# Kernel optimization log

Hardware: AMD Instinct MI355X
Metric: run time of the kernel (lower is better)

Reference implementation:

```python
import jax, jax.numpy as jnp
import numpy as np

WS = 16      # window size
NH = 8       # num heads
LN_EPS = 1e-5
F_NORM_EPS = 1e-12  # torch F.normalize eps


def layer_norm(x, w, b):
    mu = jnp.mean(x, axis=-1, keepdims=True)
    var = jnp.mean((x - mu) ** 2, axis=-1, keepdims=True)
    return (x - mu) / jnp.sqrt(var + LN_EPS) * w + b


def setup_inputs() -> dict:
    key = jax.random.key(0)
    ks = jax.random.split(key, 8)
    b, h, w, c = 2, 192, 192, 128
    n = WS * WS
    x = jax.random.normal(ks[0], (b, h * w, c), dtype=jnp.float32)
    rpi = jax.random.randint(ks[1], (n, n), 0, (2 * WS - 1) ** 2)
    s = 0.02
    inp = {
        'x': x,
        'qkv_w': jax.random.normal(ks[2], (c, 3 * c), jnp.float32) * s,
        'qkv_b': jnp.zeros((3 * c,), jnp.float32),
        'proj_w': jax.random.normal(ks[3], (c, c), jnp.float32) * s,
        'proj_b': jnp.zeros((c,), jnp.float32),
        'logit_scale': jnp.full((NH, 1, 1), jnp.log(10.0), jnp.float32),
        'rpb_table': jax.random.normal(ks[4], ((2 * WS - 1) ** 2, NH), jnp.float32) * s,
        'norm1_w': jnp.ones((c,), jnp.float32),
        'norm1_b': jnp.zeros((c,), jnp.float32),
        'norm2_w': jnp.ones((c,), jnp.float32),
        'norm2_b': jnp.zeros((c,), jnp.float32),
        'fc1_w': jax.random.normal(ks[5], (c, 2 * c), jnp.float32) * s,
        'fc1_b': jnp.zeros((2 * c,), jnp.float32),
        'fc2_w': jax.random.normal(ks[6], (2 * c, c), jnp.float32) * s,
        'fc2_b': jnp.zeros((c,), jnp.float32),
        'h': h,
        'w': w,
        'rpi': rpi,
    }
    return inp


def reference(x, qkv_w, qkv_b, proj_w, proj_b, logit_scale, rpb_table,
              norm1_w, norm1_b, norm2_w, norm2_b, fc1_w, fc1_b, fc2_w, fc2_b,
              h, w, rpi):
    b, L, c = x.shape
    ws, nh = WS, NH
    d = c // nh
    n = ws * ws
    shortcut = x

    # window partition: (b, h, w, c) -> (b*nW, ws*ws, c)
    xi = x.reshape(b, h // ws, ws, w // ws, ws, c)
    xw = xi.transpose(0, 1, 3, 2, 4, 5).reshape(-1, n, c)

    # cosine window attention (SwinV2 style)
    qkv = (xw @ qkv_w + qkv_b).reshape(-1, n, 3, nh, d).transpose(2, 0, 3, 1, 4)
    q, k, v = qkv[0], qkv[1], qkv[2]                       # (B_, nh, n, d)
    qn = q / jnp.maximum(jnp.linalg.norm(q, axis=-1, keepdims=True), F_NORM_EPS)
    kn = k / jnp.maximum(jnp.linalg.norm(k, axis=-1, keepdims=True), F_NORM_EPS)
    scale = jnp.exp(jnp.minimum(logit_scale, jnp.log(100.0)))  # (nh,1,1)
    attn = jnp.einsum('bhnd,bhmd->bhnm', qn, kn) * scale
    bias = rpb_table[rpi.reshape(-1)].reshape(n, n, nh).transpose(2, 0, 1)
    attn = jax.nn.softmax(attn + bias[None], axis=-1)
    out = jnp.einsum('bhnm,bhmd->bhnd', attn, v)
    out = out.transpose(0, 2, 1, 3).reshape(-1, n, c) @ proj_w + proj_b

    # window reverse
    xr = out.reshape(b, h // ws, w // ws, ws, ws, c)
    xr = xr.transpose(0, 1, 3, 2, 4, 5).reshape(b, L, c)

    # res-post-norm residual + MLP (GELU), eval mode (no dropout/drop_path)
    x1 = shortcut + layer_norm(xr, norm1_w, norm1_b)
    y = jax.nn.gelu(x1 @ fc1_w + fc1_b, approximate=False) @ fc2_w + fc2_b
    return x1 + layer_norm(y, norm2_w, norm2_b)
```

## Files before the change

kernel.cpp:

```cpp
#include <hip/hip_runtime.h>
#include <hip/hip_bf16.h>
#include <math.h>

#define BB 2
#define HH 192
#define WW 192
#define CC 128
#define LL (HH*WW)
#define WSZ 16
#define NTOK 256
#define NHEAD 8
#define DHEAD 16
#define NWS 12
#define NWB 144
#define NWT 288
#define MT (BB*LL)
#define LOG2E 1.44269504088896340736f

#define OFF_BIAS   0
#define OFF_QKV    262144
#define OFF_ATTN   14417920
#define OFF_X1     19136512
#define OFF_X1B    28573696
#define OFF_HID    33292288
#define OFF_WT     42729472
#define WT_QKV 0
#define WT_PROJ 49152
#define WT_FC1 65536
#define WT_FC2 98304

typedef short  bf16x8  __attribute__((ext_vector_type(8)));
typedef short  bf16x4  __attribute__((ext_vector_type(4)));
typedef float  f32x4   __attribute__((ext_vector_type(4)));
typedef float  f32x16  __attribute__((ext_vector_type(16)));
typedef uint   uint4v  __attribute__((ext_vector_type(4)));
#define MFMA16(a,b,c) __builtin_amdgcn_mfma_f32_16x16x32_bf16(a,b,c,0,0,0)
#define MFMA32(a,b,c) __builtin_amdgcn_mfma_f32_32x32x16_bf16(a,b,c,0,0,0)

__device__ __forceinline__ ushort f2b(float f) {
    uint u = __float_as_uint(f);
    uint r = u + 0x7fffu + ((u >> 16) & 1u);
    return (ushort)(r >> 16);
}
__device__ __forceinline__ uint pk(float a, float b) {
    return (uint)f2b(a) | ((uint)f2b(b) << 16);
}
__device__ __forceinline__ float b2f(ushort u) {
    return __uint_as_float(((uint)u) << 16);
}

__device__ __forceinline__ int win_to_g(int wi, int t) {
    int b   = wi / NWB;
    int win = wi - b*NWB;
    int hi  = win / NWS;
    int wj  = win - hi*NWS;
    return b*LL + (hi*WSZ + (t >> 4))*WW + wj*WSZ + (t & 15);
}

__global__ __launch_bounds__(256) void bias_kernel(const int* __restrict__ rpi,
                                                   const float* __restrict__ rpb,
                                                   ushort* __restrict__ biasT) {
    int gid = blockIdx.x*256 + threadIdx.x;
    int q = gid >> 8, k = gid & 255;
    int idx = rpi[q*256 + k];
    #pragma unroll
    for (int h = 0; h < 8; ++h)
        biasT[h*65536 + q*256 + k] = f2b(rpb[idx*8 + h] * LOG2E);
}

__global__ __launch_bounds__(256) void wconv_kernel(const float* __restrict__ qkv_w,
                                                    const float* __restrict__ proj_w,
                                                    const float* __restrict__ fc1_w,
                                                    const float* __restrict__ fc2_w,
                                                    ushort* __restrict__ wt) {
    int gid = blockIdx.x*256 + threadIdx.x;
    if (gid < 49152) {
        int n = gid >> 7, k = gid & 127;
        wt[gid] = f2b(qkv_w[k*384 + n]);
    } else if (gid < 65536) {
        int i = gid - 49152; int n = i >> 7, k = i & 127;
        wt[gid] = f2b(proj_w[k*128 + n]);
    } else if (gid < 98304) {
        int i = gid - 65536; int n = i >> 7, k = i & 127;
        wt[gid] = f2b(fc1_w[k*256 + n]);
    } else {
        int i = gid - 98304; int n = i >> 8, k = i & 255;
        wt[gid] = f2b(fc2_w[k*128 + n]);
    }
}

__global__ __launch_bounds__(256) void qkv_mfma(const float* __restrict__ x,
                                                const ushort* __restrict__ wt,
                                                const float* __restrict__ wb,
                                                const float* __restrict__ lscale,
                                                ushort* __restrict__ qkvbuf) {
    __shared__ ushort alds[128][136];
    const int tid = threadIdx.x;
    const int wi  = blockIdx.x >> 1;
    const int t0w = (blockIdx.x & 1) << 7;
    #pragma unroll
    for (int it = 0; it < 16; ++it) {
        int idx = it*256 + tid;
        int row = idx >> 5, c4 = idx & 31;
        int g = win_to_g(wi, t0w + row);
        float4 v = ((const float4*)x)[g*32 + c4];
        ushort4 b;
        b.x = f2b(v.x); b.y = f2b(v.y); b.z = f2b(v.z); b.w = f2b(v.w);
        *(ushort4*)&alds[row][c4*4] = b;
    }
    __syncthreads();
    const int wv = tid >> 6, lane = tid & 63;
    const int lr = lane & 15, kg = lane >> 4;
    bf16x8 af[2][4];
    #pragma unroll
    for (int mt = 0; mt < 2; ++mt)
        #pragma unroll
        for (int ks = 0; ks < 4; ++ks)
            af[mt][ks] = *(const bf16x8*)&alds[wv*32 + mt*16 + lr][ks*32 + kg*8];

    #pragma unroll 4
    for (int t = 0; t < 24; ++t) {
        bf16x8 bfr[4];
        #pragma unroll
        for (int ks = 0; ks < 4; ++ks)
            bfr[ks] = *(const bf16x8*)(wt + (t*16 + lr)*128 + ks*32 + kg*8);
        f32x4 acc[2];
        acc[0] = (f32x4)0.f; acc[1] = (f32x4)0.f;
        #pragma unroll
        for (int mt = 0; mt < 2; ++mt)
            #pragma unroll
            for (int ks = 0; ks < 4; ++ks)
                acc[mt] = MFMA16(af[mt][ks], bfr[ks], acc[mt]);

        const int s = t >> 3, head = t & 7;
        const float bcol = wb[s*128 + head*16 + lr];
        #pragma unroll
        for (int mt = 0; mt < 2; ++mt)
            #pragma unroll
            for (int r = 0; r < 4; ++r) acc[mt][r] += bcol;
        if (s < 2) {
            float sc = (s == 0) ? __expf(fminf(lscale[head], 4.6051701860f)) * LOG2E : 1.f;
            #pragma unroll
            for (int mt = 0; mt < 2; ++mt)
                #pragma unroll
                for (int r = 0; r < 4; ++r) {
                    float ss = acc[mt][r]*acc[mt][r];
                    ss += __shfl_xor(ss, 1);
                    ss += __shfl_xor(ss, 2);
                    ss += __shfl_xor(ss, 4);
                    ss += __shfl_xor(ss, 8);
                    acc[mt][r] *= sc / fmaxf(sqrtf(ss), 1e-12f);
                }
        }
        ushort* dst = qkvbuf + ((wi*8+head)*3 + s)*4096;
        #pragma unroll
        for (int mt = 0; mt < 2; ++mt)
            #pragma unroll
            for (int r = 0; r < 4; ++r) {
                int row = t0w + wv*32 + mt*16 + kg*4 + r;
                dst[row*16 + lr] = f2b(acc[mt][r]);
            }
    }
}

__global__ __launch_bounds__(256) void attn_mfma(const ushort* __restrict__ qkv,
                                                 const ushort* __restrict__ biasT,
                                                 ushort* __restrict__ attn_o) {
    __shared__ ushort Vt[16][260];
    __shared__ float  ltab[4][2][32];
    const int tid = threadIdx.x;
    const int wi = blockIdx.x >> 3, head = blockIdx.x & 7;
    const ushort* qb = qkv + ((wi*8 + head)*3)*4096;
    const ushort* kb = qb + 4096;
    const ushort* vb = qb + 8192;
    {
        const ushort* vr = vb + tid*16;
        #pragma unroll
        for (int c = 0; c < 4; ++c) {
            ushort4 vv = *(const ushort4*)(vr + c*4);
            Vt[c*4+0][tid] = vv.x; Vt[c*4+1][tid] = vv.y;
            Vt[c*4+2][tid] = vv.z; Vt[c*4+3][tid] = vv.w;
        }
    }
    const int wv = tid >> 6, lane = tid & 63;
    const int l31 = lane & 31, hi = lane >> 5;
    const int dp = l31 & 15;
    bf16x8 qf[2];
    #pragma unroll
    for (int mt = 0; mt < 2; ++mt)
        qf[mt] = *(const bf16x8*)(qb + (wv*64 + mt*32 + l31)*16 + hi*8);
    const ushort* brow0 = biasT + head*65536 + (wv*64 + l31)*256;
    __syncthreads();

    f32x16 oacc[2];
    oacc[0] = (f32x16)0.f; oacc[1] = (f32x16)0.f;
    float lsum0 = 0.f, lsum1 = 0.f;

    for (int kt = 0; kt < 8; ++kt) {
        bf16x8 kf = *(const bf16x8*)(kb + (kt*32 + l31)*16 + hi*8);
        #pragma unroll
        for (int mt = 0; mt < 2; ++mt) {
            f32x16 s = MFMA32(kf, qf[mt], (f32x16)0.f);
            const ushort* br = brow0 + mt*32*256 + kt*32 + 4*hi;
            ushort4 b0 = *(const ushort4*)(br + 0);
            ushort4 b1 = *(const ushort4*)(br + 8);
            ushort4 b2 = *(const ushort4*)(br + 16);
            ushort4 b3 = *(const ushort4*)(br + 24);
            float p[16];
            p[0]  = exp2f(s[0]  + b2f(b0.x));
            p[1]  = exp2f(s[1]  + b2f(b0.y));
            p[2]  = exp2f(s[2]  + b2f(b0.z));
            p[3]  = exp2f(s[3]  + b2f(b0.w));
            p[4]  = exp2f(s[4]  + b2f(b1.x));
            p[5]  = exp2f(s[5]  + b2f(b1.y));
            p[6]  = exp2f(s[6]  + b2f(b1.z));
            p[7]  = exp2f(s[7]  + b2f(b1.w));
            p[8]  = exp2f(s[8]  + b2f(b2.x));
            p[9]  = exp2f(s[9]  + b2f(b2.y));
            p[10] = exp2f(s[10] + b2f(b2.z));
            p[11] = exp2f(s[11] + b2f(b2.w));
            p[12] = exp2f(s[12] + b2f(b3.x));
            p[13] = exp2f(s[13] + b2f(b3.y));
            p[14] = exp2f(s[14] + b2f(b3.z));
            p[15] = exp2f(s[15] + b2f(b3.w));
            float ls = ((p[0]+p[1])+(p[2]+p[3])) + ((p[4]+p[5])+(p[6]+p[7]))
                     + ((p[8]+p[9])+(p[10]+p[11])) + ((p[12]+p[13])+(p[14]+p[15]));
            if (mt == 0) lsum0 += ls; else lsum1 += ls;
            uint4v t0 = { pk(p[0],p[1]),  pk(p[2],p[3]),  pk(p[4],p[5]),  pk(p[6],p[7])  };
            uint4v t1 = { pk(p[8],p[9]),  pk(p[10],p[11]),pk(p[12],p[13]),pk(p[14],p[15])};
            bf16x8 pf0 = __builtin_bit_cast(bf16x8, t0);
            bf16x8 pf1 = __builtin_bit_cast(bf16x8, t1);
            bf16x4 v00 = *(const bf16x4*)&Vt[dp][kt*32 + hi*4];
            bf16x4 v01 = *(const bf16x4*)&Vt[dp][kt*32 + 8 + hi*4];
            bf16x4 v10 = *(const bf16x4*)&Vt[dp][kt*32 + 16 + hi*4];
            bf16x4 v11 = *(const bf16x4*)&Vt[dp][kt*32 + 24 + hi*4];
            bf16x8 vf0 = __builtin_shufflevector(v00, v01, 0,1,2,3,4,5,6,7);
            bf16x8 vf1 = __builtin_shufflevector(v10, v11, 0,1,2,3,4,5,6,7);
            oacc[mt] = MFMA32(pf0, vf0, oacc[mt]);
            oacc[mt] = MFMA32(pf1, vf1, oacc[mt]);
        }
    }
    {
        float t0 = lsum0 + __shfl_xor(lsum0, 32);
        float t1 = lsum1 + __shfl_xor(lsum1, 32);
        ltab[wv][0][l31] = 1.f / t0;
        ltab[wv][1][l31] = 1.f / t1;
    }
    __syncthreads();
    if (l31 < 16) {
        #pragma unroll
        for (int mt = 0; mt < 2; ++mt) {
            #pragma unroll
            for (int i = 0; i < 16; ++i) {
                int q = (i&3) + 8*(i>>2) + 4*hi;
                float il = ltab[wv][mt][q];
                attn_o[(wi*256 + wv*64 + mt*32 + q)*128 + head*16 + l31]
                    = f2b(oacc[mt][i] * il);
            }
        }
    }
}

__global__ __launch_bounds__(256) void proj_mfma(const ushort* __restrict__ a,
                                                 const ushort* __restrict__ wt,
                                                 const float* __restrict__ wb,
                                                 const float* __restrict__ x,
                                                 const float* __restrict__ n1w,
                                                 const float* __restrict__ n1b,
                                                 float* __restrict__ x1,
                                                 ushort* __restrict__ x1b) {
    __shared__ ushort alds[128][136];
    const int tid = threadIdx.x;
    const int M0 = blockIdx.x * 128;
    #pragma unroll
    for (int it = 0; it < 16; ++it) {
        int idx = it*256 + tid;
        int row = idx >> 5, c4 = idx & 31;
        *(ushort4*)&alds[row][c4*4] = ((const ushort4*)a)[M0*32 + idx];
    }
    __syncthreads();
    const int wv = tid >> 6, lane = tid & 63;
    const int lr = lane & 15, kg = lane >> 4;
    bf16x8 af[2][4];
    #pragma unroll
    for (int mt = 0; mt < 2; ++mt)
        #pragma unroll
        for (int ks = 0; ks < 4; ++ks)
            af[mt][ks] = *(const bf16x8*)&alds[wv*32 + mt*16 + lr][ks*32 + kg*8];

    f32x4 acc[2][8];
    #pragma unroll
    for (int mt = 0; mt < 2; ++mt)
        #pragma unroll
        for (int t = 0; t < 8; ++t) acc[mt][t] = (f32x4)0.f;
    #pragma unroll
    for (int t = 0; t < 8; ++t) {
        bf16x8 bfr[4];
        #pragma unroll
        for (int ks = 0; ks < 4; ++ks)
            bfr[ks] = *(const bf16x8*)(wt + (t*16 + lr)*128 + ks*32 + kg*8);
        #pragma unroll
        for (int mt = 0; mt < 2; ++mt)
            #pragma unroll
            for (int ks = 0; ks < 4; ++ks)
                acc[mt][t] = MFMA16(af[mt][ks], bfr[ks], acc[mt][t]);
    }
    #pragma unroll
    for (int t = 0; t < 8; ++t) {
        float bcol = wb[t*16 + lr];
        #pragma unroll
        for (int mt = 0; mt < 2; ++mt)
            #pragma unroll
            for (int r = 0; r < 4; ++r) acc[mt][t][r] += bcol;
    }
    float mu_[2][4], rs_[2][4];
    #pragma unroll
    for (int mt = 0; mt < 2; ++mt)
        #pragma unroll
        for (int r = 0; r < 4; ++r) {
            float s = 0.f, q = 0.f;
            #pragma unroll
            for (int t = 0; t < 8; ++t) { float v = acc[mt][t][r]; s += v; q += v*v; }
            s += __shfl_xor(s,1); q += __shfl_xor(q,1);
            s += __shfl_xor(s,2); q += __shfl_xor(q,2);
            s += __shfl_xor(s,4); q += __shfl_xor(q,4);
            s += __shfl_xor(s,8); q += __shfl_xor(q,8);
            float mu = s*(1.f/128.f);
            float var = q*(1.f/128.f) - mu*mu;
            mu_[mt][r] = mu; rs_[mt][r] = rsqrtf(var + 1e-5f);
        }
    float w1c[8], b1c[8];
    #pragma unroll
    for (int t = 0; t < 8; ++t) { w1c[t] = n1w[t*16+lr]; b1c[t] = n1b[t*16+lr]; }
    #pragma unroll
    for (int mt = 0; mt < 2; ++mt)
        #pragma unroll
        for (int r = 0; r < 4; ++r) {
            int M = M0 + wv*32 + mt*16 + kg*4 + r;
            int g = win_to_g(M >> 8, M & 255);
            #pragma unroll
            for (int t = 0; t < 8; ++t) {
                int col = t*16 + lr;
                float val = x[g*128 + col]
                          + (acc[mt][t][r]-mu_[mt][r])*rs_[mt][r]*w1c[t] + b1c[t];
                x1[g*128 + col] = val;
                x1b[g*128 + col] = f2b(val);
            }
        }
}

__global__ __launch_bounds__(256) void fc1_mfma(const ushort* __restrict__ a,
                                                const ushort* __restrict__ wt,
                                                const float* __restrict__ wb,
                                                ushort* __restrict__ hidden) {
    __shared__ ushort alds[128][136];
    const int tid = threadIdx.x;
    const int M0 = blockIdx.x * 128;
    #pragma unroll
    for (int it = 0; it < 16; ++it) {
        int idx = it*256 + tid;
        int row = idx >> 5, c4 = idx & 31;
        *(ushort4*)&alds[row][c4*4] = ((const ushort4*)a)[M0*32 + idx];
    }
    __syncthreads();
    const int wv = tid >> 6, lane = tid & 63;
    const int lr = lane & 15, kg = lane >> 4;
    bf16x8 af[2][4];
    #pragma unroll
    for (int mt = 0; mt < 2; ++mt)
        #pragma unroll
        for (int ks = 0; ks < 4; ++ks)
            af[mt][ks] = *(const bf16x8*)&alds[wv*32 + mt*16 + lr][ks*32 + kg*8];

    #pragma unroll 4
    for (int t = 0; t < 16; ++t) {
        bf16x8 bfr[4];
        #pragma unroll
        for (int ks = 0; ks < 4; ++ks)
            bfr[ks] = *(const bf16x8*)(wt + (t*16 + lr)*128 + ks*32 + kg*8);
        f32x4 acc[2];
        acc[0] = (f32x4)0.f; acc[1] = (f32x4)0.f;
        #pragma unroll
        for (int mt = 0; mt < 2; ++mt)
            #pragma unroll
            for (int ks = 0; ks < 4; ++ks)
                acc[mt] = MFMA16(af[mt][ks], bfr[ks], acc[mt]);
        float bcol = wb[t*16 + lr];
        int col = t*16 + lr;
        #pragma unroll
        for (int mt = 0; mt < 2; ++mt)
            #pragma unroll
            for (int r = 0; r < 4; ++r) {
                int row = M0 + wv*32 + mt*16 + kg*4 + r;
                float v = acc[mt][r] + bcol;
                float gl = v*0.5f*(1.f + erff(v*0.70710678118654752f));
                hidden[row*256 + col] = f2b(gl);
            }
    }
}

__global__ __launch_bounds__(256) void fc2_mfma(const ushort* __restrict__ a,
                                                const ushort* __restrict__ wt,
                                                const float* __restrict__ wb,
                                                const float* __restrict__ x1,
                                                const float* __restrict__ n2w,
                                                const float* __restrict__ n2b,
                                                float* __restrict__ out) {
    __shared__ ushort alds[128][136];
    const int tid = threadIdx.x;
    const int M0 = blockIdx.x * 128;
    const int wv = tid >> 6, lane = tid & 63;
    const int lr = lane & 15, kg = lane >> 4;
    f32x4 acc[2][8];
    #pragma unroll
    for (int mt = 0; mt < 2; ++mt)
        #pragma unroll
        for (int t = 0; t < 8; ++t) acc[mt][t] = (f32x4)0.f;

    for (int ko = 0; ko < 2; ++ko) {
        if (ko) __syncthreads();
        #pragma unroll
        for (int it = 0; it < 16; ++it) {
            int idx = it*256 + tid;
            int row = idx >> 5, c4 = idx & 31;
            *(ushort4*)&alds[row][c4*4] =
                *(const ushort4*)(a + (M0+row)*256 + ko*128 + c4*4);
        }
        __syncthreads();
        bf16x8 af[2][4];
        #pragma unroll
        for (int mt = 0; mt < 2; ++mt)
            #pragma unroll
            for (int ks = 0; ks < 4; ++ks)
                af[mt][ks] = *(const bf16x8*)&alds[wv*32 + mt*16 + lr][ks*32 + kg*8];
        #pragma unroll
        for (int t = 0; t < 8; ++t) {
            bf16x8 bfr[4];
            #pragma unroll
            for (int ks = 0; ks < 4; ++ks)
                bfr[ks] = *(const bf16x8*)(wt + (t*16 + lr)*256 + ko*128 + ks*32 + kg*8);
            #pragma unroll
            for (int mt = 0; mt < 2; ++mt)
                #pragma unroll
                for (int ks = 0; ks < 4; ++ks)
                    acc[mt][t] = MFMA16(af[mt][ks], bfr[ks], acc[mt][t]);
        }
    }
    #pragma unroll
    for (int t = 0; t < 8; ++t) {
        float bcol = wb[t*16 + lr];
        #pragma unroll
        for (int mt = 0; mt < 2; ++mt)
            #pragma unroll
            for (int r = 0; r < 4; ++r) acc[mt][t][r] += bcol;
    }
    float mu_[2][4], rs_[2][4];
    #pragma unroll
    for (int mt = 0; mt < 2; ++mt)
        #pragma unroll
        for (int r = 0; r < 4; ++r) {
            float s = 0.f, q = 0.f;
            #pragma unroll
            for (int t = 0; t < 8; ++t) { float v = acc[mt][t][r]; s += v; q += v*v; }
            s += __shfl_xor(s,1); q += __shfl_xor(q,1);
            s += __shfl_xor(s,2); q += __shfl_xor(q,2);
            s += __shfl_xor(s,4); q += __shfl_xor(q,4);
            s += __shfl_xor(s,8); q += __shfl_xor(q,8);
            float mu = s*(1.f/128.f);
            float var = q*(1.f/128.f) - mu*mu;
            mu_[mt][r] = mu; rs_[mt][r] = rsqrtf(var + 1e-5f);
        }
    float w2c[8], b2c[8];
    #pragma unroll
    for (int t = 0; t < 8; ++t) { w2c[t] = n2w[t*16+lr]; b2c[t] = n2b[t*16+lr]; }
    #pragma unroll
    for (int mt = 0; mt < 2; ++mt)
        #pragma unroll
        for (int r = 0; r < 4; ++r) {
            int g = M0 + wv*32 + mt*16 + kg*4 + r;
            #pragma unroll
            for (int t = 0; t < 8; ++t) {
                int col = t*16 + lr;
                out[g*128 + col] = x1[g*128 + col]
                                 + (acc[mt][t][r]-mu_[mt][r])*rs_[mt][r]*w2c[t] + b2c[t];
            }
        }
}

extern "C" void kernel_launch(void* const* d_in, const int* in_sizes, int n_in,
                              void* d_out, int out_size, void* d_ws, size_t ws_size,
                              hipStream_t stream) {
    const float* x      = (const float*)d_in[0];
    const float* qkv_w  = (const float*)d_in[1];
    const float* qkv_b  = (const float*)d_in[2];
    const float* proj_w = (const float*)d_in[3];
    const float* proj_b = (const float*)d_in[4];
    const float* lscale = (const float*)d_in[5];
    const float* rpb    = (const float*)d_in[6];
    const float* n1w    = (const float*)d_in[7];
    const float* n1b    = (const float*)d_in[8];
    const float* n2w    = (const float*)d_in[9];
    const float* n2b    = (const float*)d_in[10];
    const float* fc1_w  = (const float*)d_in[11];
    const float* fc1_b  = (const float*)d_in[12];
    const float* fc2_w  = (const float*)d_in[13];
    const float* fc2_b  = (const float*)d_in[14];
    const int*   rpi    = (const int*)d_in[17];
    float* out = (float*)d_out;

    float* ws      = (float*)d_ws;
    ushort* biasT  = (ushort*)(ws + OFF_BIAS);
    ushort* qkvbuf = (ushort*)(ws + OFF_QKV);
    ushort* attn_o = (ushort*)(ws + OFF_ATTN);
    float*  x1     = ws + OFF_X1;
    ushort* x1b    = (ushort*)(ws + OFF_X1B);
    ushort* hidden = (ushort*)(ws + OFF_HID);
    ushort* wt     = (ushort*)(ws + OFF_WT);

    bias_kernel<<<256, 256, 0, stream>>>(rpi, rpb, biasT);
    wconv_kernel<<<512, 256, 0, stream>>>(qkv_w, proj_w, fc1_w, fc2_w, wt);
    qkv_mfma<<<576, 256, 0, stream>>>(x, wt + WT_QKV, qkv_b, lscale, qkvbuf);
    attn_mfma<<<2304, 256, 0, stream>>>(qkvbuf, biasT, attn_o);
    proj_mfma<<<576, 256, 0, stream>>>(attn_o, wt + WT_PROJ, proj_b, x, n1w, n1b, x1, x1b);
    fc1_mfma<<<576, 256, 0, stream>>>(x1b, wt + WT_FC1, fc1_b, hidden);
    fc2_mfma<<<576, 256, 0, stream>>>(hidden, wt + WT_FC2, fc2_b, x1, n2w, n2b, out);
}
```

Baseline: 353.1 us.

## Fold bias into MFMA accumulator, compute row sums via ones-column, use hardware bf16 pack

The relative-position bias is now stored in fp32 and passed as the initial accumulator of the QK^T MFMA, which removes the per-element bias add. The softmax denominator is no longer summed on the VALU. A constant row of ones is appended to the V tile, so the idle upper lanes of the PV MFMA produce the row sums, which are then shuffled back to the output lanes. This also removes the LDS table and a barrier. Float-to-bf16 conversion switches to the v_cvt_pk_bf16_f32 instruction. In exchange the bias buffer is twice as large, so the attention kernel reads more global memory.

```diff
diff --git a/kernel.cpp b/kernel.cpp
--- a/kernel.cpp
+++ b/kernel.cpp
@@ -18,12 +18,12 @@
 #define LOG2E 1.44269504088896340736f
 
 #define OFF_BIAS   0
-#define OFF_QKV    262144
-#define OFF_ATTN   14417920
-#define OFF_X1     19136512
-#define OFF_X1B    28573696
-#define OFF_HID    33292288
-#define OFF_WT     42729472
+#define OFF_QKV    524288
+#define OFF_ATTN   14680064
+#define OFF_X1     19398656
+#define OFF_X1B    28835840
+#define OFF_HID    33554432
+#define OFF_WT     42991616
 #define WT_QKV 0
 #define WT_PROJ 49152
 #define WT_FC1 65536
@@ -37,13 +37,15 @@
 #define MFMA16(a,b,c) __builtin_amdgcn_mfma_f32_16x16x32_bf16(a,b,c,0,0,0)
 #define MFMA32(a,b,c) __builtin_amdgcn_mfma_f32_32x32x16_bf16(a,b,c,0,0,0)
 
+__device__ __forceinline__ uint cvtpk(float a, float b) {
+    uint r;
+    asm("v_cvt_pk_bf16_f32 %0, %1, %2" : "=v"(r) : "v"(a), "v"(b));
+    return r;
+}
 __device__ __forceinline__ ushort f2b(float f) {
-    uint u = __float_as_uint(f);
-    uint r = u + 0x7fffu + ((u >> 16) & 1u);
-    return (ushort)(r >> 16);
-}
-__device__ __forceinline__ uint pk(float a, float b) {
-    return (uint)f2b(a) | ((uint)f2b(b) << 16);
+    uint r;
+    asm("v_cvt_pk_bf16_f32 %0, %1, %1" : "=v"(r) : "v"(f));
+    return (ushort)r;
 }
 __device__ __forceinline__ float b2f(ushort u) {
     return __uint_as_float(((uint)u) << 16);
@@ -59,13 +61,13 @@
 
 __global__ __launch_bounds__(256) void bias_kernel(const int* __restrict__ rpi,
                                                    const float* __restrict__ rpb,
-                                                   ushort* __restrict__ biasT) {
+                                                   float* __restrict__ biasT) {
     int gid = blockIdx.x*256 + threadIdx.x;
     int q = gid >> 8, k = gid & 255;
     int idx = rpi[q*256 + k];
     #pragma unroll
     for (int h = 0; h < 8; ++h)
-        biasT[h*65536 + q*256 + k] = f2b(rpb[idx*8 + h] * LOG2E);
+        biasT[h*65536 + q*256 + k] = rpb[idx*8 + h] * LOG2E;
 }
 
 __global__ __launch_bounds__(256) void wconv_kernel(const float* __restrict__ qkv_w,
@@ -104,9 +106,10 @@
         int row = idx >> 5, c4 = idx & 31;
         int g = win_to_g(wi, t0w + row);
         float4 v = ((const float4*)x)[g*32 + c4];
-        ushort4 b;
-        b.x = f2b(v.x); b.y = f2b(v.y); b.z = f2b(v.z); b.w = f2b(v.w);
-        *(ushort4*)&alds[row][c4*4] = b;
+        uint2 pkd;
+        pkd.x = cvtpk(v.x, v.y);
+        pkd.y = cvtpk(v.z, v.w);
+        *(uint2*)&alds[row][c4*4] = pkd;
     }
     __syncthreads();
     const int wv = tid >> 6, lane = tid & 63;
@@ -164,10 +167,9 @@
 }
 
 __global__ __launch_bounds__(256) void attn_mfma(const ushort* __restrict__ qkv,
-                                                 const ushort* __restrict__ biasT,
+                                                 const float* __restrict__ biasT,
                                                  ushort* __restrict__ attn_o) {
-    __shared__ ushort Vt[16][260];
-    __shared__ float  ltab[4][2][32];
+    __shared__ ushort Vt[17][260];
     const int tid = threadIdx.x;
     const int wi = blockIdx.x >> 3, head = blockIdx.x & 7;
     const ushort* qb = qkv + ((wi*8 + head)*3)*4096;
@@ -181,53 +183,40 @@
             Vt[c*4+0][tid] = vv.x; Vt[c*4+1][tid] = vv.y;
             Vt[c*4+2][tid] = vv.z; Vt[c*4+3][tid] = vv.w;
         }
+        Vt[16][tid] = 0x3F80;
     }
     const int wv = tid >> 6, lane = tid & 63;
     const int l31 = lane & 31, hi = lane >> 5;
-    const int dp = l31 & 15;
+    const int dp = (l31 < 16) ? l31 : 16;
     bf16x8 qf[2];
     #pragma unroll
     for (int mt = 0; mt < 2; ++mt)
         qf[mt] = *(const bf16x8*)(qb + (wv*64 + mt*32 + l31)*16 + hi*8);
-    const ushort* brow0 = biasT + head*65536 + (wv*64 + l31)*256;
+    const float* brow0 = biasT + head*65536 + (wv*64 + l31)*256 + 4*hi;
     __syncthreads();
 
     f32x16 oacc[2];
     oacc[0] = (f32x16)0.f; oacc[1] = (f32x16)0.f;
-    float lsum0 = 0.f, lsum1 = 0.f;
 
     for (int kt = 0; kt < 8; ++kt) {
         bf16x8 kf = *(const bf16x8*)(kb + (kt*32 + l31)*16 + hi*8);
         #pragma unroll
         for (int mt = 0; mt < 2; ++mt) {
-            f32x16 s = MFMA32(kf, qf[mt], (f32x16)0.f);
-            const ushort* br = brow0 + mt*32*256 + kt*32 + 4*hi;
-            ushort4 b0 = *(const ushort4*)(br + 0);
-            ushort4 b1 = *(const ushort4*)(br + 8);
-            ushort4 b2 = *(const ushort4*)(br + 16);
-            ushort4 b3 = *(const ushort4*)(br + 24);
+            const float* br = brow0 + mt*8192 + kt*32;
+            float4 b0 = *(const float4*)(br);
+            float4 b1 = *(const float4*)(br + 8);
+            float4 b2 = *(const float4*)(br + 16);
+            float4 b3 = *(const float4*)(br + 24);
+            f32x16 ci = { b0.x,b0.y,b0.z,b0.w, b1.x,b1.y,b1.z,b1.w,
+                          b2.x,b2.y,b2.z,b2.w, b3.x,b3.y,b3.z,b3.w };
+            f32x16 s = MFMA32(kf, qf[mt], ci);
             float p[16];
-            p[0]  = exp2f(s[0]  + b2f(b0.x));
-            p[1]  = exp2f(s[1]  + b2f(b0.y));
-            p[2]  = exp2f(s[2]  + b2f(b0.z));
-            p[3]  = exp2f(s[3]  + b2f(b0.w));
-            p[4]  = exp2f(s[4]  + b2f(b1.x));
-            p[5]  = exp2f(s[5]  + b2f(b1.y));
-            p[6]  = exp2f(s[6]  + b2f(b1.z));
-            p[7]  = exp2f(s[7]  + b2f(b1.w));
-            p[8]  = exp2f(s[8]  + b2f(b2.x));
-            p[9]  = exp2f(s[9]  + b2f(b2.y));
-            p[10] = exp2f(s[10] + b2f(b2.z));
-            p[11] = exp2f(s[11] + b2f(b2.w));
-            p[12] = exp2f(s[12] + b2f(b3.x));
-            p[13] = exp2f(s[13] + b2f(b3.y));
-            p[14] = exp2f(s[14] + b2f(b3.z));
-            p[15] = exp2f(s[15] + b2f(b3.w));
-            float ls = ((p[0]+p[1])+(p[2]+p[3])) + ((p[4]+p[5])+(p[6]+p[7]))
-                     + ((p[8]+p[9])+(p[10]+p[11])) + ((p[12]+p[13])+(p[14]+p[15]));
-            if (mt == 0) lsum0 += ls; else lsum1 += ls;
-            uint4v t0 = { pk(p[0],p[1]),  pk(p[2],p[3]),  pk(p[4],p[5]),  pk(p[6],p[7])  };
-            uint4v t1 = { pk(p[8],p[9]),  pk(p[10],p[11]),pk(p[12],p[13]),pk(p[14],p[15])};
+            #pragma unroll
+            for (int i = 0; i < 16; ++i) p[i] = exp2f(s[i]);
+            uint4v t0 = { cvtpk(p[0],p[1]),   cvtpk(p[2],p[3]),
+                          cvtpk(p[4],p[5]),   cvtpk(p[6],p[7]) };
+            uint4v t1 = { cvtpk(p[8],p[9]),   cvtpk(p[10],p[11]),
+                          cvtpk(p[12],p[13]), cvtpk(p[14],p[15]) };
             bf16x8 pf0 = __builtin_bit_cast(bf16x8, t0);
             bf16x8 pf1 = __builtin_bit_cast(bf16x8, t1);
             bf16x4 v00 = *(const bf16x4*)&Vt[dp][kt*32 + hi*4];
@@ -240,20 +229,18 @@
             oacc[mt] = MFMA32(pf1, vf1, oacc[mt]);
         }
     }
-    {
-        float t0 = lsum0 + __shfl_xor(lsum0, 32);
-        float t1 = lsum1 + __shfl_xor(lsum1, 32);
-        ltab[wv][0][l31] = 1.f / t0;
-        ltab[wv][1][l31] = 1.f / t1;
-    }
-    __syncthreads();
-    if (l31 < 16) {
-        #pragma unroll
-        for (int mt = 0; mt < 2; ++mt) {
-            #pragma unroll
-            for (int i = 0; i < 16; ++i) {
+    #pragma unroll
+    for (int mt = 0; mt < 2; ++mt) {
+        f32x16 o = oacc[mt];
+        if (l31 >= 16) {
+            #pragma unroll
+            for (int i = 0; i < 16; ++i) o[i] = __builtin_amdgcn_rcpf(o[i]);
+        }
+        #pragma unroll
+        for (int i = 0; i < 16; ++i) {
+            float il = __shfl(o[i], (lane & 32) + 16);
+            if (l31 < 16) {
                 int q = (i&3) + 8*(i>>2) + 4*hi;
-                float il = ltab[wv][mt][q];
                 attn_o[(wi*256 + wv*64 + mt*32 + q)*128 + head*16 + l31]
                     = f2b(oacc[mt][i] * il);
             }
@@ -509,7 +496,7 @@
     float* out = (float*)d_out;
 
     float* ws      = (float*)d_ws;
-    ushort* biasT  = (ushort*)(ws + OFF_BIAS);
+    float*  biasT  = ws + OFF_BIAS;
     ushort* qkvbuf = (ushort*)(ws + OFF_QKV);
     ushort* attn_o = (ushort*)(ws + OFF_ATTN);
     float*  x1     = ws + OFF_X1;
```

New measurement: 351.8 us. Within noise of the previous version (-0.4%).
